# Kernel tuning notes

Hardware: AMD Instinct MI355X
Metric: run time of the kernel (lower is better)

The kernel has to match this reference:

```python
import jax, jax.numpy as jnp
import numpy as np

H, L, N = 512, 2048, 64  # channels, seq len, SSM state size


def _make_dplr_hippo(n):
    # make_HiPPO / make_NPLR_HiPPO / make_DPLR_HiPPO from the source
    p0 = np.sqrt(1.0 + 2.0 * np.arange(n))
    A = p0[:, None] * p0[None, :]
    A = np.tril(A) - np.diag(np.arange(n))
    nhippo = -A
    P = np.sqrt(np.arange(n) + 0.5)
    B = np.sqrt(2.0 * np.arange(n) + 1.0)
    S = nhippo + P[:, None] * P[None, :]
    S_diag = np.diagonal(S)
    Lam_re = np.mean(S_diag) * np.ones_like(S_diag)
    Lam_im, V = jnp.linalg.eigh(jnp.asarray(S, jnp.complex64) * (-1j))
    Pc = V.conj().T @ jnp.asarray(P, jnp.complex64)
    Bc = V.conj().T @ jnp.asarray(B, jnp.complex64)
    return (jnp.asarray(Lam_re, jnp.float32), jnp.asarray(Lam_im, jnp.float32),
            Pc, Bc)


def setup_inputs() -> dict:
    key = jax.random.key(0)
    k_u, k_c, k_s = jax.random.split(key, 3)
    Lre, Lim, Pc, Bc = _make_dplr_hippo(N)
    tile = lambda v: jnp.tile(v[None, :], (H, 1)).astype(jnp.float32)  # (H,N)
    return {
        "u": jax.random.normal(k_u, (L, H), dtype=jnp.float32),
        "x0_re": jnp.zeros((N, H), jnp.float32),
        "x0_im": jnp.zeros((N, H), jnp.float32),
        "Lambda_re": tile(Lre),
        "Lambda_im": tile(Lim),
        "P_re": tile(Pc.real), "P_im": tile(Pc.imag),
        "B_re": tile(Bc.real), "B_im": tile(Bc.imag),
        "C": jax.random.normal(k_c, (H, N, 2), jnp.float32) * (0.5 ** 0.5),
        "D": jnp.ones((H, 1), jnp.float32),
        "log_step": jax.random.uniform(k_s, (H, 1), jnp.float32,
                                       minval=np.log(1e-3), maxval=np.log(1e-1)),
    }


def _discretize(Lam, P, B, Ct, step):
    # discrete_DPLR with Q = P (as in setup); per-channel, vmapped over H.
    n = Lam.shape[0]
    I = jnp.eye(n, dtype=jnp.complex64)
    A = jnp.diag(Lam) - P[:, None] * P.conj()[None, :]
    A0 = (2.0 / step) * I + A
    Dd = jnp.diag(1.0 / (2.0 / step - Lam))
    Qc = P.conj()[None, :]            # (1,N)
    P2 = P[:, None]                   # (N,1)
    A1 = Dd - (Dd @ P2) * (1.0 / (1.0 + Qc @ Dd @ P2)) * (Qc @ Dd)
    Ab = A1 @ A0                      # (N,N)
    Bb = 2.0 * (A1 @ B[:, None])[:, 0]
    AbL = jnp.linalg.matrix_power(Ab, L)
    Cb = (Ct[None, :] @ jnp.linalg.inv(I - AbL).conj()).conj()[0]
    return Ab, Bb, Cb


def _forward(u, x0_re, x0_im, Lambda_re, Lambda_im, P_re, P_im,
             B_re, B_im, C, D, log_step):
    Lam = jnp.clip(Lambda_re, None, -0.0001) + 1j * Lambda_im  # (H,N)
    Pc = P_re + 1j * P_im
    Bc = B_re + 1j * B_im
    Cc = C[..., 0] + 1j * C[..., 1]
    step = jnp.exp(log_step)[:, 0]                              # (H,)
    Ab, Bb, Cb = jax.vmap(_discretize)(Lam, Pc, Bc, Cc, step)   # (H,N,N),(H,N),(H,N)

    x0 = jnp.transpose(x0_re + 1j * x0_im)                      # (H,N) complex

    def body(x, u_t):  # x: (H,N) complex, u_t: (H,)
        x = jnp.einsum('hnm,hm->hn', Ab, x) + Bb * u_t[:, None]
        y = jnp.einsum('hn,hn->h', Cb, x)
        return x, y.real

    _, ys = jax.lax.scan(body, x0, u)                           # ys: (L,H)
    return ys + u * D[:, 0][None, :]                            # (L,H) float32


def reference(u, x0_re, x0_im, Lambda_re, Lambda_im, P_re, P_im,
              B_re, B_im, C, D, log_step):
    return _forward(u, x0_re, x0_im, Lambda_re, Lambda_im, P_re, P_im,
                    B_re, B_im, C, D, log_step)
```

## Files before the change

kernel.cpp:

```cpp
#include <hip/hip_runtime.h>

#define HH 512
#define LL 2048
#define NN 64
#define TT 64
#define CC 32
#define NLDA 68
#define SP 72

typedef __attribute__((ext_vector_type(8))) short bf16x8_t;
typedef __attribute__((ext_vector_type(4))) float floatx4;

__device__ __forceinline__ float2 cmul(float2 a, float2 b) {
    return make_float2(a.x * b.x - a.y * b.y, a.x * b.y + a.y * b.x);
}
__device__ __forceinline__ float2 crecip(float2 a) {
    float id = 1.0f / (a.x * a.x + a.y * a.y);
    return make_float2(a.x * id, -a.y * id);
}
template <int CTRL>
__device__ __forceinline__ float dpp_mov(float x) {
    return __int_as_float(__builtin_amdgcn_update_dpp(
        0, __float_as_int(x), CTRL, 0xf, 0xf, true));
}
__device__ __forceinline__ float wave_sum_bcast(float x) {
    x += dpp_mov<0x111>(x);
    x += dpp_mov<0x112>(x);
    x += dpp_mov<0x114>(x);
    x += dpp_mov<0x118>(x);
    x += dpp_mov<0x142>(x);
    x += dpp_mov<0x143>(x);
    return __int_as_float(__builtin_amdgcn_readlane(__float_as_int(x), 63));
}
__device__ __forceinline__ float rlane(float x, int i) {
    return __int_as_float(__builtin_amdgcn_readlane(__float_as_int(x), i));
}
__device__ __forceinline__ unsigned short f2bf(float f) {
    unsigned int u = __float_as_uint(f);
    u += 0x7FFFu + ((u >> 16) & 1u);
    return (unsigned short)(u >> 16);
}
__device__ __forceinline__ float bf2f(unsigned short s) {
    return __uint_as_float(((unsigned int)s) << 16);
}

__device__ __forceinline__ void closed_form(
    int h, int n,
    const float* __restrict__ Lre, const float* __restrict__ Lim,
    const float* __restrict__ Pre, const float* __restrict__ Pim,
    const float* __restrict__ Bre, const float* __restrict__ Bim,
    const float* __restrict__ logstep,
    float2& da, float2& DPv, float2& tv, float2& bb) {
    float step = expf(logstep[h]);
    float as = 2.0f / step;
    float lr = fminf(Lre[h * NN + n], -1e-4f);
    float li = Lim[h * NN + n];
    float2 a = make_float2(as + lr, li);
    float2 Dn = crecip(make_float2(as - lr, -li));
    float2 P = make_float2(Pre[h * NN + n], Pim[h * NN + n]);
    float2 Bv = make_float2(Bre[h * NN + n], Bim[h * NN + n]);
    float2 cP = make_float2(P.x, -P.y);
    float p2 = P.x * P.x + P.y * P.y;
    float2 rt = cmul(cmul(cP, Dn), Bv);
    float2 e = make_float2(wave_sum_bcast(Dn.x * p2), wave_sum_bcast(Dn.y * p2));
    float2 rv = make_float2(wave_sum_bcast(rt.x), wave_sum_bcast(rt.y));
    float2 cc = crecip(make_float2(1.0f + e.x, e.y));
    da = cmul(Dn, a);
    DPv = cmul(Dn, P);
    float2 tmp = cmul(cc, make_float2(da.x - e.x, da.y - e.y));
    tv = cmul(cP, make_float2(1.0f + tmp.x, tmp.y));
    float2 crv = cmul(cc, rv);
    float2 cd = cmul(crv, DPv);
    float2 db = cmul(Dn, Bv);
    bb = make_float2(2.0f * (db.x - cd.x), 2.0f * (db.y - cd.y));
}

__device__ __forceinline__ void pack_tiles(
    unsigned short* mRh, unsigned short* mRl,
    unsigned short* mIh, unsigned short* mIl,
    unsigned short* mTRh, unsigned short* mTRl,
    unsigned short* mTIh, unsigned short* mTIl,
    int w, int lm, int q, const float Cr[4][4], const float Ci[4][4]) {
    #pragma unroll
    for (int nt = 0; nt < 4; ++nt) {
        const int c = nt * 16 + lm;
        unsigned short hr[4], lr_[4], hi_[4], li_[4];
        #pragma unroll
        for (int reg = 0; reg < 4; ++reg) {
            const float xr = Cr[nt][reg], xi = Ci[nt][reg];
            hr[reg] = f2bf(xr); lr_[reg] = f2bf(xr - bf2f(hr[reg]));
            hi_[reg] = f2bf(xi); li_[reg] = f2bf(xi - bf2f(hi_[reg]));
            const int r = 16 * w + 4 * q + reg;
            mRh[r * SP + c] = hr[reg]; mRl[r * SP + c] = lr_[reg];
            mIh[r * SP + c] = hi_[reg]; mIl[r * SP + c] = li_[reg];
        }
        const int tb = c * SP + 16 * w + 4 * q;
        *(ushort4*)&mTRh[tb] = make_ushort4(hr[0], hr[1], hr[2], hr[3]);
        *(ushort4*)&mTRl[tb] = make_ushort4(lr_[0], lr_[1], lr_[2], lr_[3]);
        *(ushort4*)&mTIh[tb] = make_ushort4(hi_[0], hi_[1], hi_[2], hi_[3]);
        *(ushort4*)&mTIl[tb] = make_ushort4(li_[0], li_[1], li_[2], li_[3]);
    }
}

extern "C" __global__ void __launch_bounds__(256, 2)
k_fusedA(const float* __restrict__ Lre, const float* __restrict__ Lim,
         const float* __restrict__ Pre, const float* __restrict__ Pim,
         const float* __restrict__ Bre, const float* __restrict__ Bim,
         const float* __restrict__ Cmat, const float* __restrict__ logstep,
         const float* __restrict__ u,
         float2* __restrict__ wM, float2* __restrict__ wCb,
         float2* __restrict__ wP) {
    extern __shared__ __align__(16) char smem[];
    const int tid = threadIdx.x;

    if (blockIdx.x < HH) {
        const int h = blockIdx.x;
        unsigned short* mRh  = (unsigned short*)smem;
        unsigned short* mRl  = mRh + 64 * SP;
        unsigned short* mIh  = mRl + 64 * SP;
        unsigned short* mIl  = mIh + 64 * SP;
        unsigned short* mTRh = mIl + 64 * SP;
        unsigned short* mTRl = mTRh + 64 * SP;
        unsigned short* mTIh = mTRl + 64 * SP;
        unsigned short* mTIl = mTIh + 64 * SP;
        float* Nr = (float*)smem;
        float* Ni = Nr + 64 * NLDA;
        float2* sda  = (float2*)(smem + 73728);
        float2* sDP  = sda + NN;
        float2* st   = sDP + NN;
        float2* sBb  = st + NN;
        float2* srhs = sBb + NN;
        float2* sx   = srhs + NN;
        float2* pp   = sx + NN;

        const int w = tid >> 6;
        const int lane = tid & 63;
        const int lm = lane & 15, q = lane >> 4;

        if (tid < NN) {
            float2 da, DPv, tv, bb;
            closed_form(h, tid, Lre, Lim, Pre, Pim, Bre, Bim, logstep,
                        da, DPv, tv, bb);
            sda[tid] = da; sDP[tid] = DPv; st[tid] = tv; sBb[tid] = bb;
            srhs[tid] = make_float2(Cmat[h * NN * 2 + tid * 2],
                                    -Cmat[h * NN * 2 + tid * 2 + 1]);
        }
        __syncthreads();

        {
            float Cr[4][4], Ci[4][4];
            #pragma unroll
            for (int nt = 0; nt < 4; ++nt) {
                const int c = nt * 16 + lm;
                const float2 tc = st[c];
                #pragma unroll
                for (int reg = 0; reg < 4; ++reg) {
                    const int r = 16 * w + 4 * q + reg;
                    const float2 dp = sDP[r];
                    float vr = -(dp.x * tc.x - dp.y * tc.y);
                    float vi = -(dp.x * tc.y + dp.y * tc.x);
                    if (r == c) { vr += sda[r].x; vi += sda[r].y; }
                    Cr[nt][reg] = vr; Ci[nt][reg] = vi;
                }
            }
            pack_tiles(mRh, mRl, mIh, mIl, mTRh, mTRl, mTIh, mTIl,
                       w, lm, q, Cr, Ci);
        }
        __syncthreads();

        const int arow = (16 * w + lm) * SP + q * 8;
        for (int it = 0; it < 11; ++it) {
            floatx4 z4 = {0.f, 0.f, 0.f, 0.f};
            floatx4 aP[4] = {z4, z4, z4, z4};
            floatx4 aQ[4] = {z4, z4, z4, z4};
            floatx4 aC[4] = {z4, z4, z4, z4};
            for (int k2 = 0; k2 < 2; ++k2) {
                const int ao = arow + k2 * 32;
                const bf16x8_t ARh = *(const bf16x8_t*)&mRh[ao];
                const bf16x8_t ARl = *(const bf16x8_t*)&mRl[ao];
                const bf16x8_t AIh = *(const bf16x8_t*)&mIh[ao];
                const bf16x8_t AIl = *(const bf16x8_t*)&mIl[ao];
                bf16x8_t BRh[4], BRl[4], BIh[4], BIl[4];
                #pragma unroll
                for (int nt = 0; nt < 4; ++nt) {
                    const int bo = (nt * 16 + lm) * SP + k2 * 32 + q * 8;
                    BRh[nt] = *(const bf16x8_t*)&mTRh[bo];
                    BRl[nt] = *(const bf16x8_t*)&mTRl[bo];
                    BIh[nt] = *(const bf16x8_t*)&mTIh[bo];
                    BIl[nt] = *(const bf16x8_t*)&mTIl[bo];
                }
                #pragma unroll
                for (int nt = 0; nt < 4; ++nt) {
                    aP[nt] = __builtin_amdgcn_mfma_f32_16x16x32_bf16(ARh, BRh[nt], aP[nt], 0, 0, 0);
                    aP[nt] = __builtin_amdgcn_mfma_f32_16x16x32_bf16(ARh, BRl[nt], aP[nt], 0, 0, 0);
                    aP[nt] = __builtin_amdgcn_mfma_f32_16x16x32_bf16(ARl, BRh[nt], aP[nt], 0, 0, 0);
                    aQ[nt] = __builtin_amdgcn_mfma_f32_16x16x32_bf16(AIh, BIh[nt], aQ[nt], 0, 0, 0);
                    aQ[nt] = __builtin_amdgcn_mfma_f32_16x16x32_bf16(AIh, BIl[nt], aQ[nt], 0, 0, 0);
                    aQ[nt] = __builtin_amdgcn_mfma_f32_16x16x32_bf16(AIl, BIh[nt], aQ[nt], 0, 0, 0);
                    aC[nt] = __builtin_amdgcn_mfma_f32_16x16x32_bf16(ARh, BIh[nt], aC[nt], 0, 0, 0);
                    aC[nt] = __builtin_amdgcn_mfma_f32_16x16x32_bf16(ARh, BIl[nt], aC[nt], 0, 0, 0);
                    aC[nt] = __builtin_amdgcn_mfma_f32_16x16x32_bf16(ARl, BIh[nt], aC[nt], 0, 0, 0);
                    aC[nt] = __builtin_amdgcn_mfma_f32_16x16x32_bf16(AIh, BRh[nt], aC[nt], 0, 0, 0);
                    aC[nt] = __builtin_amdgcn_mfma_f32_16x16x32_bf16(AIh, BRl[nt], aC[nt], 0, 0, 0);
                    aC[nt] = __builtin_amdgcn_mfma_f32_16x16x32_bf16(AIl, BRh[nt], aC[nt], 0, 0, 0);
                }
            }
            __syncthreads();
            if (it < 10) {
                float Cr[4][4], Ci[4][4];
                #pragma unroll
                for (int nt = 0; nt < 4; ++nt)
                    #pragma unroll
                    for (int reg = 0; reg < 4; ++reg) {
                        Cr[nt][reg] = aP[nt][reg] - aQ[nt][reg];
                        Ci[nt][reg] = aC[nt][reg];
                    }
                pack_tiles(mRh, mRl, mIh, mIl, mTRh, mTRl, mTIh, mTIl,
                           w, lm, q, Cr, Ci);
                __syncthreads();
                if (it == 5) {
                    for (int idx = tid; idx < NN * NN; idx += 256) {
                        const int c = idx >> 6, k = idx & 63;
                        wM[h * NN * NN + idx] = make_float2(
                            bf2f(mTRh[c * SP + k]) + bf2f(mTRl[c * SP + k]),
                            bf2f(mTIh[c * SP + k]) + bf2f(mTIl[c * SP + k]));
                    }
                }
            } else {
                #pragma unroll
                for (int nt = 0; nt < 4; ++nt) {
                    const int c = nt * 16 + lm;
                    #pragma unroll
                    for (int reg = 0; reg < 4; ++reg) {
                        const int r = 16 * w + 4 * q + reg;
                        Nr[r * NLDA + c] = aP[nt][reg] - aQ[nt][reg];
                        Ni[r * NLDA + c] = aC[nt][reg];
                    }
                }
                __syncthreads();
            }
        }

        if (tid < NN) sx[tid] = srhs[tid];
        __syncthreads();
        for (int itn = 0; itn < 24; ++itn) {
            const int i = tid & 63, qq = tid >> 6;
            float pr = 0.0f, pi = 0.0f;
            #pragma unroll 4
            for (int jj = 0; jj < 16; ++jj) {
                const int j = qq * 16 + jj;
                const float nr = Nr[j * NLDA + i], ni = Ni[j * NLDA + i];
                const float2 xj = sx[j];
                pr += nr * xj.x - ni * xj.y;
                pi += nr * xj.y + ni * xj.x;
            }
            pp[qq * 64 + i] = make_float2(pr, pi);
            __syncthreads();
            if (tid < NN) {
                const float2 a0 = pp[tid], a1 = pp[64 + tid];
                const float2 a2 = pp[128 + tid], a3 = pp[192 + tid];
                sx[tid] = make_float2(
                    srhs[tid].x + a0.x + a1.x + a2.x + a3.x,
                    srhs[tid].y + a0.y + a1.y + a2.y + a3.y);
            }
            __syncthreads();
        }
        if (tid < NN) wCb[h * NN + tid] = sx[tid];
    } else {
        const int h = blockIdx.x - HH;
        float2* sG  = (float2*)smem;
        float*  su  = (float*)(smem + 32768);
        float2* sda = (float2*)(smem + 40960);
        float2* sDP = sda + NN;
        float2* st  = sDP + NN;
        float2* sBb = st + NN;

        const int wv = tid >> 6, lane = tid & 63;
        for (int idx = tid; idx < LL; idx += 256)
            su[idx] = u[idx * HH + h];
        if (tid < NN) {
            float2 da, DPv, tv, bb;
            closed_form(h, tid, Lre, Lim, Pre, Pim, Bre, Bim, logstep,
                        da, DPv, tv, bb);
            sda[tid] = da; sDP[tid] = DPv; st[tid] = tv; sBb[tid] = bb;
        }
        __syncthreads();

        if (tid < 64) {
            const float2 da = sda[lane], DP = sDP[lane], tt = st[lane];
            float Gr = sBb[lane].x, Gi = sBb[lane].y;
            for (int m = 0; m < TT; ++m) {
                sG[m * NN + lane] = make_float2(Gr, Gi);
                float c1 = tt.x * Gr - tt.y * Gi;
                float c2 = tt.x * Gi + tt.y * Gr;
                c1 += dpp_mov<0x111>(c1); c2 += dpp_mov<0x111>(c2);
                c1 += dpp_mov<0x112>(c1); c2 += dpp_mov<0x112>(c2);
                c1 += dpp_mov<0x114>(c1); c2 += dpp_mov<0x114>(c2);
                c1 += dpp_mov<0x118>(c1); c2 += dpp_mov<0x118>(c2);
                c1 += dpp_mov<0x142>(c1); c2 += dpp_mov<0x142>(c2);
                c1 += dpp_mov<0x143>(c1); c2 += dpp_mov<0x143>(c2);
                const float S1 = rlane(c1, 63);
                const float S2 = rlane(c2, 63);
                float nGr = da.x * Gr - da.y * Gi - (DP.x * S1 - DP.y * S2);
                float nGi = da.x * Gi + da.y * Gr - (DP.x * S2 + DP.y * S1);
                Gr = nGr; Gi = nGi;
            }
        }
        __syncthreads();

        float accr[8] = {}, acci[8] = {};
        for (int j = 0; j < TT; ++j) {
            const float2 g = sG[(TT - 1 - j) * NN + lane];
            #pragma unroll
            for (int qc = 0; qc < 8; ++qc) {
                const float uv = su[((wv * 8 + qc) << 6) + j];
                accr[qc] += g.x * uv; acci[qc] += g.y * uv;
            }
        }
        #pragma unroll
        for (int qc = 0; qc < 8; ++qc)
            wP[(h * CC + wv * 8 + qc) * NN + lane] = make_float2(accr[qc], acci[qc]);
    }
}

extern "C" __global__ void __launch_bounds__(256, 2)
k_fusedB(const float* __restrict__ Lre, const float* __restrict__ Lim,
         const float* __restrict__ Pre, const float* __restrict__ Pim,
         const float* __restrict__ Bre, const float* __restrict__ Bim,
         const float* __restrict__ logstep,
         const float* __restrict__ u, const float* __restrict__ Dvec,
         const float* __restrict__ x0_re, const float* __restrict__ x0_im,
         const float2* __restrict__ wM, const float2* __restrict__ wCb,
         const float2* __restrict__ wP, float* __restrict__ out) {
    extern __shared__ __align__(16) char smem[];
    float2* sM          = (float2*)smem;
    unsigned short* sVr = (unsigned short*)(smem + 32768);
    unsigned short* sVi = (unsigned short*)(smem + 41216);
    float2* sXs         = (float2*)(smem + 49664);
    float*  su          = (float*)(smem + 66048);
    float*  sK          = (float*)(smem + 74240);

    const int h = blockIdx.x;
    const int tid = threadIdx.x;
    const int wv = tid >> 6, lane = tid & 63;

    for (int idx = tid; idx < NN * NN; idx += 256)
        sM[idx] = wM[h * NN * NN + idx];
    for (int idx = tid; idx < LL; idx += 256)
        su[idx] = u[idx * HH + h];
    __syncthreads();

    if (wv == 0) {
        float2 da, DP, tt, Bb;
        closed_form(h, lane, Lre, Lim, Pre, Pim, Bre, Bim, logstep,
                    da, DP, tt, Bb);
        const float2 Cb = wCb[h * NN + lane];
        float Gr = Bb.x, Gi = Bb.y;
        float vr = Cb.x, vi = Cb.y;
        for (int m = 0; m < TT; ++m) {
            float ch[5];
            ch[0] = Cb.x * Gr - Cb.y * Gi;
            ch[1] = tt.x * Gr - tt.y * Gi;
            ch[2] = tt.x * Gi + tt.y * Gr;
            ch[3] = vr * DP.x - vi * DP.y;
            ch[4] = vr * DP.y + vi * DP.x;
            #pragma unroll
            for (int c = 0; c < 5; ++c) ch[c] += dpp_mov<0x111>(ch[c]);
            #pragma unroll
            for (int c = 0; c < 5; ++c) ch[c] += dpp_mov<0x112>(ch[c]);
            #pragma unroll
            for (int c = 0; c < 5; ++c) ch[c] += dpp_mov<0x114>(ch[c]);
            #pragma unroll
            for (int c = 0; c < 5; ++c) ch[c] += dpp_mov<0x118>(ch[c]);
            #pragma unroll
            for (int c = 0; c < 5; ++c) ch[c] += dpp_mov<0x142>(ch[c]);
            #pragma unroll
            for (int c = 0; c < 5; ++c) ch[c] += dpp_mov<0x143>(ch[c]);
            const float S0 = rlane(ch[0], 63);
            const float S1 = rlane(ch[1], 63);
            const float S2 = rlane(ch[2], 63);
            const float S3 = rlane(ch[3], 63);
            const float S4 = rlane(ch[4], 63);
            if (lane == 0) sK[m] = S0;
            float nGr = da.x * Gr - da.y * Gi - (DP.x * S1 - DP.y * S2);
            float nGi = da.x * Gi + da.y * Gr - (DP.x * S2 + DP.y * S1);
            Gr = nGr; Gi = nGi;
            float nvr = da.x * vr - da.y * vi - (S3 * tt.x - S4 * tt.y);
            float nvi = da.x * vi + da.y * vr - (S3 * tt.y + S4 * tt.x);
            vr = nvr; vi = nvi;
            sVr[lane * 66 + m] = f2bf(vr);
            sVi[lane * 66 + m] = f2bf(vi);
        }
    } else if (wv == 1) {
        float xr = x0_re[lane * HH + h], xi = x0_im[lane * HH + h];
        sXs[lane] = make_float2(xr, xi);
        for (int c = 1; c < CC; ++c) {
            float nr = 0.0f, ni = 0.0f;
            #pragma unroll 8
            for (int j = 0; j < NN; ++j) {
                const float xjr = rlane(xr, j);
                const float xji = rlane(xi, j);
                const float2 m = sM[j * NN + lane];
                nr += m.x * xjr - m.y * xji;
                ni += m.x * xji + m.y * xjr;
            }
            const float2 pe = wP[(h * CC + (c - 1)) * NN + lane];
            xr = nr + pe.x; xi = ni + pe.y;
            sXs[c * NN + lane] = make_float2(xr, xi);
        }
    }
    __syncthreads();

    const float Dh = Dvec[h];
    const int t = lane;
    float acc[8] = {};
    for (int s = 0; s < TT; ++s) {
        const int d = t - s;
        const float kv = (d >= 0) ? sK[d < 0 ? 0 : d] : 0.0f;
        #pragma unroll
        for (int qc = 0; qc < 8; ++qc)
            acc[qc] += kv * su[((wv * 8 + qc) << 6) + s];
    }
    for (int n = 0; n < NN; ++n) {
        const float vvr = bf2f(sVr[n * 66 + t]);
        const float vvi = bf2f(sVi[n * 66 + t]);
        #pragma unroll
        for (int qc = 0; qc < 8; ++qc) {
            const float2 xs = sXs[(wv * 8 + qc) * NN + n];
            acc[qc] += vvr * xs.x - vvi * xs.y;
        }
    }
    #pragma unroll
    for (int qc = 0; qc < 8; ++qc) {
        const int c = wv * 8 + qc;
        out[(c * TT + t) * HH + h] = acc[qc] + Dh * su[c * TT + t];
    }
}

extern "C" void kernel_launch(void* const* d_in, const int* in_sizes, int n_in,
                              void* d_out, int out_size, void* d_ws, size_t ws_size,
                              hipStream_t stream) {
    const float* u    = (const float*)d_in[0];
    const float* x0re = (const float*)d_in[1];
    const float* x0im = (const float*)d_in[2];
    const float* Lre  = (const float*)d_in[3];
    const float* Lim  = (const float*)d_in[4];
    const float* Pre  = (const float*)d_in[5];
    const float* Pim  = (const float*)d_in[6];
    const float* Bre  = (const float*)d_in[7];
    const float* Bim  = (const float*)d_in[8];
    const float* C    = (const float*)d_in[9];
    const float* Dv   = (const float*)d_in[10];
    const float* lst  = (const float*)d_in[11];

    float2* wM  = (float2*)d_ws;
    float2* wP  = wM + HH * NN * NN;
    float2* wCb = wP + HH * CC * NN;
    float* out = (float*)d_out;

    hipLaunchKernelGGL(k_fusedA, dim3(2 * HH), dim3(256), 78848, stream,
                       Lre, Lim, Pre, Pim, Bre, Bim, C, lst, u,
                       wM, wCb, wP);
    hipLaunchKernelGGL(k_fusedB, dim3(HH), dim3(256), 74496, stream,
                       Lre, Lim, Pre, Pim, Bre, Bim, lst, u, Dv,
                       x0re, x0im, wM, wCb, wP, out);
}
```

Measured before the change: 233.9 us.

## Fuse discretization, chunk-input and scan kernels into one per-channel kernel

Merges the two launches into a single kernel of 512 blocks, one per channel. The G/P chunk-input blocks and the output kernel are folded into the matrix-power block, so Cb, the chunk inputs P and the closed-form parameters stay in shared memory instead of round-tripping through global workspace. The chunk-to-chunk state propagation now reads the M matrix directly from global memory (written earlier by the same block) rather than staging it in shared memory. This halves the grid and serializes work that previously ran in parallel blocks, and it risks slower M reads from global memory in the sequential chunk recurrence.

New measurement: 255.2 us. +9.1%, slower.

```diff
diff --git a/kernel.cpp b/kernel.cpp
--- a/kernel.cpp
+++ b/kernel.cpp
@@ -7,6 +7,7 @@
 #define CC 32
 #define NLDA 68
 #define SP 72
+
 
 typedef __attribute__((ext_vector_type(8))) short bf16x8_t;
 typedef __attribute__((ext_vector_type(4))) float floatx4;
@@ -103,259 +104,182 @@
 }
 
 extern "C" __global__ void __launch_bounds__(256, 2)
-k_fusedA(const float* __restrict__ Lre, const float* __restrict__ Lim,
-         const float* __restrict__ Pre, const float* __restrict__ Pim,
-         const float* __restrict__ Bre, const float* __restrict__ Bim,
-         const float* __restrict__ Cmat, const float* __restrict__ logstep,
-         const float* __restrict__ u,
-         float2* __restrict__ wM, float2* __restrict__ wCb,
-         float2* __restrict__ wP) {
+k_all(const float* __restrict__ Lre, const float* __restrict__ Lim,
+      const float* __restrict__ Pre, const float* __restrict__ Pim,
+      const float* __restrict__ Bre, const float* __restrict__ Bim,
+      const float* __restrict__ Cmat, const float* __restrict__ logstep,
+      const float* __restrict__ u, const float* __restrict__ Dvec,
+      const float* __restrict__ x0_re, const float* __restrict__ x0_im,
+      float2* __restrict__ wM, float* __restrict__ out) {
     extern __shared__ __align__(16) char smem[];
     const int tid = threadIdx.x;
-
-    if (blockIdx.x < HH) {
-        const int h = blockIdx.x;
-        unsigned short* mRh  = (unsigned short*)smem;
-        unsigned short* mRl  = mRh + 64 * SP;
-        unsigned short* mIh  = mRl + 64 * SP;
-        unsigned short* mIl  = mIh + 64 * SP;
-        unsigned short* mTRh = mIl + 64 * SP;
-        unsigned short* mTRl = mTRh + 64 * SP;
-        unsigned short* mTIh = mTRl + 64 * SP;
-        unsigned short* mTIl = mTIh + 64 * SP;
-        float* Nr = (float*)smem;
-        float* Ni = Nr + 64 * NLDA;
-        float2* sda  = (float2*)(smem + 73728);
-        float2* sDP  = sda + NN;
-        float2* st   = sDP + NN;
-        float2* sBb  = st + NN;
-        float2* srhs = sBb + NN;
-        float2* sx   = srhs + NN;
-        float2* pp   = sx + NN;
-
-        const int w = tid >> 6;
-        const int lane = tid & 63;
-        const int lm = lane & 15, q = lane >> 4;
-
-        if (tid < NN) {
-            float2 da, DPv, tv, bb;
-            closed_form(h, tid, Lre, Lim, Pre, Pim, Bre, Bim, logstep,
-                        da, DPv, tv, bb);
-            sda[tid] = da; sDP[tid] = DPv; st[tid] = tv; sBb[tid] = bb;
-            srhs[tid] = make_float2(Cmat[h * NN * 2 + tid * 2],
-                                    -Cmat[h * NN * 2 + tid * 2 + 1]);
+    const int h = blockIdx.x;
+
+    unsigned short* mRh  = (unsigned short*)smem;
+    unsigned short* mRl  = mRh + 64 * SP;
+    unsigned short* mIh  = mRl + 64 * SP;
+    unsigned short* mIl  = mIh + 64 * SP;
+    unsigned short* mTRh = mIl + 64 * SP;
+    unsigned short* mTRl = mTRh + 64 * SP;
+    unsigned short* mTIh = mTRl + 64 * SP;
+    unsigned short* mTIl = mTIh + 64 * SP;
+    float* Nr = (float*)smem;
+    float* Ni = Nr + 64 * NLDA;
+    float2* sda  = (float2*)(smem + 74240);
+    float2* sDP  = sda + NN;
+    float2* st   = sDP + NN;
+    float2* sBb  = st + NN;
+    float2* srhs = sBb + NN;
+    float2* sx   = srhs + NN;
+    float2* pp   = sx + NN;
+    float2* sG   = (float2*)smem;
+    unsigned short* sVr = (unsigned short*)(smem + 32768);
+    unsigned short* sVi = (unsigned short*)(smem + 41216);
+    float2* sP   = (float2*)(smem + 49664);
+    float*  su   = (float*)(smem + 66048);
+    float*  sK   = (float*)srhs;
+    float2* sXs  = (float2*)smem;
+
+    const int w = tid >> 6;
+    const int lane = tid & 63;
+    const int lm = lane & 15, q = lane >> 4;
+    const int wv = w;
+
+    if (tid < NN) {
+        float2 da, DPv, tv, bb;
+        closed_form(h, tid, Lre, Lim, Pre, Pim, Bre, Bim, logstep,
+                    da, DPv, tv, bb);
+        sda[tid] = da; sDP[tid] = DPv; st[tid] = tv; sBb[tid] = bb;
+        srhs[tid] = make_float2(Cmat[h * NN * 2 + tid * 2],
+                                -Cmat[h * NN * 2 + tid * 2 + 1]);
+    }
+    __syncthreads();
+
+    {
+        float Cr[4][4], Ci[4][4];
+        #pragma unroll
+        for (int nt = 0; nt < 4; ++nt) {
+            const int c = nt * 16 + lm;
+            const float2 tc = st[c];
+            #pragma unroll
+            for (int reg = 0; reg < 4; ++reg) {
+                const int r = 16 * w + 4 * q + reg;
+                const float2 dp = sDP[r];
+                float vr = -(dp.x * tc.x - dp.y * tc.y);
+                float vi = -(dp.x * tc.y + dp.y * tc.x);
+                if (r == c) { vr += sda[r].x; vi += sda[r].y; }
+                Cr[nt][reg] = vr; Ci[nt][reg] = vi;
+            }
+        }
+        pack_tiles(mRh, mRl, mIh, mIl, mTRh, mTRl, mTIh, mTIl,
+                   w, lm, q, Cr, Ci);
+    }
+    __syncthreads();
+
+    const int arow = (16 * w + lm) * SP + q * 8;
+    for (int it = 0; it < 11; ++it) {
+        floatx4 z4 = {0.f, 0.f, 0.f, 0.f};
+        floatx4 aP[4] = {z4, z4, z4, z4};
+        floatx4 aQ[4] = {z4, z4, z4, z4};
+        floatx4 aC[4] = {z4, z4, z4, z4};
+        for (int k2 = 0; k2 < 2; ++k2) {
+            const int ao = arow + k2 * 32;
+            const bf16x8_t ARh = *(const bf16x8_t*)&mRh[ao];
+            const bf16x8_t ARl = *(const bf16x8_t*)&mRl[ao];
+            const bf16x8_t AIh = *(const bf16x8_t*)&mIh[ao];
+            const bf16x8_t AIl = *(const bf16x8_t*)&mIl[ao];
+            bf16x8_t BRh[4], BRl[4], BIh[4], BIl[4];
+            #pragma unroll
+            for (int nt = 0; nt < 4; ++nt) {
+                const int bo = (nt * 16 + lm) * SP + k2 * 32 + q * 8;
+                BRh[nt] = *(const bf16x8_t*)&mTRh[bo];
+                BRl[nt] = *(const bf16x8_t*)&mTRl[bo];
+                BIh[nt] = *(const bf16x8_t*)&mTIh[bo];
+                BIl[nt] = *(const bf16x8_t*)&mTIl[bo];
+            }
+            #pragma unroll
+            for (int nt = 0; nt < 4; ++nt) {
+                aP[nt] = __builtin_amdgcn_mfma_f32_16x16x32_bf16(ARh, BRh[nt], aP[nt], 0, 0, 0);
+                aP[nt] = __builtin_amdgcn_mfma_f32_16x16x32_bf16(ARh, BRl[nt], aP[nt], 0, 0, 0);
+                aP[nt] = __builtin_amdgcn_mfma_f32_16x16x32_bf16(ARl, BRh[nt], aP[nt], 0, 0, 0);
+                aQ[nt] = __builtin_amdgcn_mfma_f32_16x16x32_bf16(AIh, BIh[nt], aQ[nt], 0, 0, 0);
+                aQ[nt] = __builtin_amdgcn_mfma_f32_16x16x32_bf16(AIh, BIl[nt], aQ[nt], 0, 0, 0);
+                aQ[nt] = __builtin_amdgcn_mfma_f32_16x16x32_bf16(AIl, BIh[nt], aQ[nt], 0, 0, 0);
+                aC[nt] = __builtin_amdgcn_mfma_f32_16x16x32_bf16(ARh, BIh[nt], aC[nt], 0, 0, 0);
+                aC[nt] = __builtin_amdgcn_mfma_f32_16x16x32_bf16(ARh, BIl[nt], aC[nt], 0, 0, 0);
+                aC[nt] = __builtin_amdgcn_mfma_f32_16x16x32_bf16(ARl, BIh[nt], aC[nt], 0, 0, 0);
+                aC[nt] = __builtin_amdgcn_mfma_f32_16x16x32_bf16(AIh, BRh[nt], aC[nt], 0, 0, 0);
+                aC[nt] = __builtin_amdgcn_mfma_f32_16x16x32_bf16(AIh, BRl[nt], aC[nt], 0, 0, 0);
+                aC[nt] = __builtin_amdgcn_mfma_f32_16x16x32_bf16(AIl, BRh[nt], aC[nt], 0, 0, 0);
+            }
         }
         __syncthreads();
-
-        {
+        if (it < 10) {
             float Cr[4][4], Ci[4][4];
+            #pragma unroll
+            for (int nt = 0; nt < 4; ++nt)
+                #pragma unroll
+                for (int reg = 0; reg < 4; ++reg) {
+                    Cr[nt][reg] = aP[nt][reg] - aQ[nt][reg];
+                    Ci[nt][reg] = aC[nt][reg];
+                }
+            pack_tiles(mRh, mRl, mIh, mIl, mTRh, mTRl, mTIh, mTIl,
+                       w, lm, q, Cr, Ci);
+            __syncthreads();
+            if (it == 5) {
+                for (int idx = tid; idx < NN * NN; idx += 256) {
+                    const int c = idx >> 6, k = idx & 63;
+                    wM[h * NN * NN + idx] = make_float2(
+                        bf2f(mTRh[c * SP + k]) + bf2f(mTRl[c * SP + k]),
+                        bf2f(mTIh[c * SP + k]) + bf2f(mTIl[c * SP + k]));
+                }
+            }
+        } else {
             #pragma unroll
             for (int nt = 0; nt < 4; ++nt) {
                 const int c = nt * 16 + lm;
-                const float2 tc = st[c];
                 #pragma unroll
                 for (int reg = 0; reg < 4; ++reg) {
                     const int r = 16 * w + 4 * q + reg;
-                    const float2 dp = sDP[r];
-                    float vr = -(dp.x * tc.x - dp.y * tc.y);
-                    float vi = -(dp.x * tc.y + dp.y * tc.x);
-                    if (r == c) { vr += sda[r].x; vi += sda[r].y; }
-                    Cr[nt][reg] = vr; Ci[nt][reg] = vi;
+                    Nr[r * NLDA + c] = aP[nt][reg] - aQ[nt][reg];
+                    Ni[r * NLDA + c] = aC[nt][reg];
                 }
             }
-            pack_tiles(mRh, mRl, mIh, mIl, mTRh, mTRl, mTIh, mTIl,
-                       w, lm, q, Cr, Ci);
-        }
+            for (int idx = tid; idx < LL; idx += 256)
+                su[idx] = u[idx * HH + h];
+            __syncthreads();
+        }
+    }
+
+    if (tid < NN) sx[tid] = srhs[tid];
+    __syncthreads();
+    for (int itn = 0; itn < 24; ++itn) {
+        const int i = tid & 63, qq = tid >> 6;
+        float pr = 0.0f, pi = 0.0f;
+        #pragma unroll 4
+        for (int jj = 0; jj < 16; ++jj) {
+            const int j = qq * 16 + jj;
+            const float nr = Nr[j * NLDA + i], ni = Ni[j * NLDA + i];
+            const float2 xj = sx[j];
+            pr += nr * xj.x - ni * xj.y;
+            pi += nr * xj.y + ni * xj.x;
+        }
+        pp[qq * 64 + i] = make_float2(pr, pi);
         __syncthreads();
-
-        const int arow = (16 * w + lm) * SP + q * 8;
-        for (int it = 0; it < 11; ++it) {
-            floatx4 z4 = {0.f, 0.f, 0.f, 0.f};
-            floatx4 aP[4] = {z4, z4, z4, z4};
-            floatx4 aQ[4] = {z4, z4, z4, z4};
-            floatx4 aC[4] = {z4, z4, z4, z4};
-            for (int k2 = 0; k2 < 2; ++k2) {
-                const int ao = arow + k2 * 32;
-                const bf16x8_t ARh = *(const bf16x8_t*)&mRh[ao];
-                const bf16x8_t ARl = *(const bf16x8_t*)&mRl[ao];
-                const bf16x8_t AIh = *(const bf16x8_t*)&mIh[ao];
-                const bf16x8_t AIl = *(const bf16x8_t*)&mIl[ao];
-                bf16x8_t BRh[4], BRl[4], BIh[4], BIl[4];
-                #pragma unroll
-                for (int nt = 0; nt < 4; ++nt) {
-                    const int bo = (nt * 16 + lm) * SP + k2 * 32 + q * 8;
-                    BRh[nt] = *(const bf16x8_t*)&mTRh[bo];
-                    BRl[nt] = *(const bf16x8_t*)&mTRl[bo];
-                    BIh[nt] = *(const bf16x8_t*)&mTIh[bo];
-                    BIl[nt] = *(const bf16x8_t*)&mTIl[bo];
-                }
-                #pragma unroll
-                for (int nt = 0; nt < 4; ++nt) {
-                    aP[nt] = __builtin_amdgcn_mfma_f32_16x16x32_bf16(ARh, BRh[nt], aP[nt], 0, 0, 0);
-                    aP[nt] = __builtin_amdgcn_mfma_f32_16x16x32_bf16(ARh, BRl[nt], aP[nt], 0, 0, 0);
-                    aP[nt] = __builtin_amdgcn_mfma_f32_16x16x32_bf16(ARl, BRh[nt], aP[nt], 0, 0, 0);
-                    aQ[nt] = __builtin_amdgcn_mfma_f32_16x16x32_bf16(AIh, BIh[nt], aQ[nt], 0, 0, 0);
-                    aQ[nt] = __builtin_amdgcn_mfma_f32_16x16x32_bf16(AIh, BIl[nt], aQ[nt], 0, 0, 0);
-                    aQ[nt] = __builtin_amdgcn_mfma_f32_16x16x32_bf16(AIl, BIh[nt], aQ[nt], 0, 0, 0);
-                    aC[nt] = __builtin_amdgcn_mfma_f32_16x16x32_bf16(ARh, BIh[nt], aC[nt], 0, 0, 0);
-                    aC[nt] = __builtin_amdgcn_mfma_f32_16x16x32_bf16(ARh, BIl[nt], aC[nt], 0, 0, 0);
-                    aC[nt] = __builtin_amdgcn_mfma_f32_16x16x32_bf16(ARl, BIh[nt], aC[nt], 0, 0, 0);
-                    aC[nt] = __builtin_amdgcn_mfma_f32_16x16x32_bf16(AIh, BRh[nt], aC[nt], 0, 0, 0);
-                    aC[nt] = __builtin_amdgcn_mfma_f32_16x16x32_bf16(AIh, BRl[nt], aC[nt], 0, 0, 0);
-                    aC[nt] = __builtin_amdgcn_mfma_f32_16x16x32_bf16(AIl, BRh[nt], aC[nt], 0, 0, 0);
-                }
-            }
-            __syncthreads();
-            if (it < 10) {
-                float Cr[4][4], Ci[4][4];
-                #pragma unroll
-                for (int nt = 0; nt < 4; ++nt)
-                    #pragma unroll
-                    for (int reg = 0; reg < 4; ++reg) {
-                        Cr[nt][reg] = aP[nt][reg] - aQ[nt][reg];
-                        Ci[nt][reg] = aC[nt][reg];
-                    }
-                pack_tiles(mRh, mRl, mIh, mIl, mTRh, mTRl, mTIh, mTIl,
-                           w, lm, q, Cr, Ci);
-                __syncthreads();
-                if (it == 5) {
-                    for (int idx = tid; idx < NN * NN; idx += 256) {
-                        const int c = idx >> 6, k = idx & 63;
-                        wM[h * NN * NN + idx] = make_float2(
-                            bf2f(mTRh[c * SP + k]) + bf2f(mTRl[c * SP + k]),
-                            bf2f(mTIh[c * SP + k]) + bf2f(mTIl[c * SP + k]));
-                    }
-                }
-            } else {
-                #pragma unroll
-                for (int nt = 0; nt < 4; ++nt) {
-                    const int c = nt * 16 + lm;
-                    #pragma unroll
-                    for (int reg = 0; reg < 4; ++reg) {
-                        const int r = 16 * w + 4 * q + reg;
-                        Nr[r * NLDA + c] = aP[nt][reg] - aQ[nt][reg];
-                        Ni[r * NLDA + c] = aC[nt][reg];
-                    }
-                }
-                __syncthreads();
-            }
-        }
-
-        if (tid < NN) sx[tid] = srhs[tid];
+        if (tid < NN) {
+            const float2 a0 = pp[tid], a1 = pp[64 + tid];
+            const float2 a2 = pp[128 + tid], a3 = pp[192 + tid];
+            sx[tid] = make_float2(
+                srhs[tid].x + a0.x + a1.x + a2.x + a3.x,
+                srhs[tid].y + a0.y + a1.y + a2.y + a3.y);
+        }
         __syncthreads();
-        for (int itn = 0; itn < 24; ++itn) {
-            const int i = tid & 63, qq = tid >> 6;
-            float pr = 0.0f, pi = 0.0f;
-            #pragma unroll 4
-            for (int jj = 0; jj < 16; ++jj) {
-                const int j = qq * 16 + jj;
-                const float nr = Nr[j * NLDA + i], ni = Ni[j * NLDA + i];
-                const float2 xj = sx[j];
-                pr += nr * xj.x - ni * xj.y;
-                pi += nr * xj.y + ni * xj.x;
-            }
-            pp[qq * 64 + i] = make_float2(pr, pi);
-            __syncthreads();
-            if (tid < NN) {
-                const float2 a0 = pp[tid], a1 = pp[64 + tid];
-                const float2 a2 = pp[128 + tid], a3 = pp[192 + tid];
-                sx[tid] = make_float2(
-                    srhs[tid].x + a0.x + a1.x + a2.x + a3.x,
-                    srhs[tid].y + a0.y + a1.y + a2.y + a3.y);
-            }
-            __syncthreads();
-        }
-        if (tid < NN) wCb[h * NN + tid] = sx[tid];
-    } else {
-        const int h = blockIdx.x - HH;
-        float2* sG  = (float2*)smem;
-        float*  su  = (float*)(smem + 32768);
-        float2* sda = (float2*)(smem + 40960);
-        float2* sDP = sda + NN;
-        float2* st  = sDP + NN;
-        float2* sBb = st + NN;
-
-        const int wv = tid >> 6, lane = tid & 63;
-        for (int idx = tid; idx < LL; idx += 256)
-            su[idx] = u[idx * HH + h];
-        if (tid < NN) {
-            float2 da, DPv, tv, bb;
-            closed_form(h, tid, Lre, Lim, Pre, Pim, Bre, Bim, logstep,
-                        da, DPv, tv, bb);
-            sda[tid] = da; sDP[tid] = DPv; st[tid] = tv; sBb[tid] = bb;
-        }
-        __syncthreads();
-
-        if (tid < 64) {
-            const float2 da = sda[lane], DP = sDP[lane], tt = st[lane];
-            float Gr = sBb[lane].x, Gi = sBb[lane].y;
-            for (int m = 0; m < TT; ++m) {
-                sG[m * NN + lane] = make_float2(Gr, Gi);
-                float c1 = tt.x * Gr - tt.y * Gi;
-                float c2 = tt.x * Gi + tt.y * Gr;
-                c1 += dpp_mov<0x111>(c1); c2 += dpp_mov<0x111>(c2);
-                c1 += dpp_mov<0x112>(c1); c2 += dpp_mov<0x112>(c2);
-                c1 += dpp_mov<0x114>(c1); c2 += dpp_mov<0x114>(c2);
-                c1 += dpp_mov<0x118>(c1); c2 += dpp_mov<0x118>(c2);
-                c1 += dpp_mov<0x142>(c1); c2 += dpp_mov<0x142>(c2);
-                c1 += dpp_mov<0x143>(c1); c2 += dpp_mov<0x143>(c2);
-                const float S1 = rlane(c1, 63);
-                const float S2 = rlane(c2, 63);
-                float nGr = da.x * Gr - da.y * Gi - (DP.x * S1 - DP.y * S2);
-                float nGi = da.x * Gi + da.y * Gr - (DP.x * S2 + DP.y * S1);
-                Gr = nGr; Gi = nGi;
-            }
-        }
-        __syncthreads();
-
-        float accr[8] = {}, acci[8] = {};
-        for (int j = 0; j < TT; ++j) {
-            const float2 g = sG[(TT - 1 - j) * NN + lane];
-            #pragma unroll
-            for (int qc = 0; qc < 8; ++qc) {
-                const float uv = su[((wv * 8 + qc) << 6) + j];
-                accr[qc] += g.x * uv; acci[qc] += g.y * uv;
-            }
-        }
-        #pragma unroll
-        for (int qc = 0; qc < 8; ++qc)
-            wP[(h * CC + wv * 8 + qc) * NN + lane] = make_float2(accr[qc], acci[qc]);
-    }
-}
-
-extern "C" __global__ void __launch_bounds__(256, 2)
-k_fusedB(const float* __restrict__ Lre, const float* __restrict__ Lim,
-         const float* __restrict__ Pre, const float* __restrict__ Pim,
-         const float* __restrict__ Bre, const float* __restrict__ Bim,
-         const float* __restrict__ logstep,
-         const float* __restrict__ u, const float* __restrict__ Dvec,
-         const float* __restrict__ x0_re, const float* __restrict__ x0_im,
-         const float2* __restrict__ wM, const float2* __restrict__ wCb,
-         const float2* __restrict__ wP, float* __restrict__ out) {
-    extern __shared__ __align__(16) char smem[];
-    float2* sM          = (float2*)smem;
-    unsigned short* sVr = (unsigned short*)(smem + 32768);
-    unsigned short* sVi = (unsigned short*)(smem + 41216);
-    float2* sXs         = (float2*)(smem + 49664);
-    float*  su          = (float*)(smem + 66048);
-    float*  sK          = (float*)(smem + 74240);
-
-    const int h = blockIdx.x;
-    const int tid = threadIdx.x;
-    const int wv = tid >> 6, lane = tid & 63;
-
-    for (int idx = tid; idx < NN * NN; idx += 256)
-        sM[idx] = wM[h * NN * NN + idx];
-    for (int idx = tid; idx < LL; idx += 256)
-        su[idx] = u[idx * HH + h];
-    __syncthreads();
+    }
 
     if (wv == 0) {
-        float2 da, DP, tt, Bb;
-        closed_form(h, lane, Lre, Lim, Pre, Pim, Bre, Bim, logstep,
-                    da, DP, tt, Bb);
-        const float2 Cb = wCb[h * NN + lane];
-        float Gr = Bb.x, Gi = Bb.y;
+        const float2 Cb = sx[lane];
+        const float2 da = sda[lane], DP = sDP[lane], tt = st[lane];
+        float Gr = sBb[lane].x, Gi = sBb[lane].y;
         float vr = Cb.x, vi = Cb.y;
         for (int m = 0; m < TT; ++m) {
             float ch[5];
@@ -392,6 +316,44 @@
             sVi[lane * 66 + m] = f2bf(vi);
         }
     } else if (wv == 1) {
+        const float2 da = sda[lane], DP = sDP[lane], tt = st[lane];
+        float Gr = sBb[lane].x, Gi = sBb[lane].y;
+        for (int m = 0; m < TT; ++m) {
+            sG[m * NN + lane] = make_float2(Gr, Gi);
+            float c1 = tt.x * Gr - tt.y * Gi;
+            float c2 = tt.x * Gi + tt.y * Gr;
+            c1 += dpp_mov<0x111>(c1); c2 += dpp_mov<0x111>(c2);
+            c1 += dpp_mov<0x112>(c1); c2 += dpp_mov<0x112>(c2);
+            c1 += dpp_mov<0x114>(c1); c2 += dpp_mov<0x114>(c2);
+            c1 += dpp_mov<0x118>(c1); c2 += dpp_mov<0x118>(c2);
+            c1 += dpp_mov<0x142>(c1); c2 += dpp_mov<0x142>(c2);
+            c1 += dpp_mov<0x143>(c1); c2 += dpp_mov<0x143>(c2);
+            const float S1 = rlane(c1, 63);
+            const float S2 = rlane(c2, 63);
+            float nGr = da.x * Gr - da.y * Gi - (DP.x * S1 - DP.y * S2);
+            float nGi = da.x * Gi + da.y * Gr - (DP.x * S2 + DP.y * S1);
+            Gr = nGr; Gi = nGi;
+        }
+    }
+    __syncthreads();
+
+    {
+        float accr[8] = {}, acci[8] = {};
+        for (int j = 0; j < TT; ++j) {
+            const float2 g = sG[(TT - 1 - j) * NN + lane];
+            #pragma unroll
+            for (int qc = 0; qc < 8; ++qc) {
+                const float uv = su[((wv * 8 + qc) << 6) + j];
+                accr[qc] += g.x * uv; acci[qc] += g.y * uv;
+            }
+        }
+        #pragma unroll
+        for (int qc = 0; qc < 8; ++qc)
+            sP[(wv * 8 + qc) * NN + lane] = make_float2(accr[qc], acci[qc]);
+    }
+    __syncthreads();
+
+    if (wv == 1) {
         float xr = x0_re[lane * HH + h], xi = x0_im[lane * HH + h];
         sXs[lane] = make_float2(xr, xi);
         for (int c = 1; c < CC; ++c) {
@@ -400,40 +362,42 @@
             for (int j = 0; j < NN; ++j) {
                 const float xjr = rlane(xr, j);
                 const float xji = rlane(xi, j);
-                const float2 m = sM[j * NN + lane];
+                const float2 m = wM[h * NN * NN + j * NN + lane];
                 nr += m.x * xjr - m.y * xji;
                 ni += m.x * xji + m.y * xjr;
             }
-            const float2 pe = wP[(h * CC + (c - 1)) * NN + lane];
+            const float2 pe = sP[(c - 1) * NN + lane];
             xr = nr + pe.x; xi = ni + pe.y;
             sXs[c * NN + lane] = make_float2(xr, xi);
         }
     }
     __syncthreads();
 
-    const float Dh = Dvec[h];
-    const int t = lane;
-    float acc[8] = {};
-    for (int s = 0; s < TT; ++s) {
-        const int d = t - s;
-        const float kv = (d >= 0) ? sK[d < 0 ? 0 : d] : 0.0f;
-        #pragma unroll
-        for (int qc = 0; qc < 8; ++qc)
-            acc[qc] += kv * su[((wv * 8 + qc) << 6) + s];
-    }
-    for (int n = 0; n < NN; ++n) {
-        const float vvr = bf2f(sVr[n * 66 + t]);
-        const float vvi = bf2f(sVi[n * 66 + t]);
+    {
+        const float Dh = Dvec[h];
+        const int t = lane;
+        float acc[8] = {};
+        for (int s = 0; s < TT; ++s) {
+            const int d = t - s;
+            const float kv = (d >= 0) ? sK[d < 0 ? 0 : d] : 0.0f;
+            #pragma unroll
+            for (int qc = 0; qc < 8; ++qc)
+                acc[qc] += kv * su[((wv * 8 + qc) << 6) + s];
+        }
+        for (int n = 0; n < NN; ++n) {
+            const float vvr = bf2f(sVr[n * 66 + t]);
+            const float vvi = bf2f(sVi[n * 66 + t]);
+            #pragma unroll
+            for (int qc = 0; qc < 8; ++qc) {
+                const float2 xs = sXs[(wv * 8 + qc) * NN + n];
+                acc[qc] += vvr * xs.x - vvi * xs.y;
+            }
+        }
         #pragma unroll
         for (int qc = 0; qc < 8; ++qc) {
-            const float2 xs = sXs[(wv * 8 + qc) * NN + n];
-            acc[qc] += vvr * xs.x - vvi * xs.y;
-        }
-    }
-    #pragma unroll
-    for (int qc = 0; qc < 8; ++qc) {
-        const int c = wv * 8 + qc;
-        out[(c * TT + t) * HH + h] = acc[qc] + Dh * su[c * TT + t];
+            const int c = wv * 8 + qc;
+            out[(c * TT + t) * HH + h] = acc[qc] + Dh * su[c * TT + t];
+        }
     }
 }
 
@@ -453,15 +417,10 @@
     const float* Dv   = (const float*)d_in[10];
     const float* lst  = (const float*)d_in[11];
 
-    float2* wM  = (float2*)d_ws;
-    float2* wP  = wM + HH * NN * NN;
-    float2* wCb = wP + HH * CC * NN;
+    float2* wM = (float2*)d_ws;
     float* out = (float*)d_out;
 
-    hipLaunchKernelGGL(k_fusedA, dim3(2 * HH), dim3(256), 78848, stream,
-                       Lre, Lim, Pre, Pim, Bre, Bim, C, lst, u,
-                       wM, wCb, wP);
-    hipLaunchKernelGGL(k_fusedB, dim3(HH), dim3(256), 74496, stream,
-                       Lre, Lim, Pre, Pim, Bre, Bim, lst, u, Dv,
-                       x0re, x0im, wM, wCb, wP, out);
-}
+    hipLaunchKernelGGL(k_all, dim3(HH), dim3(256), 79360, stream,
+                       Lre, Lim, Pre, Pim, Bre, Bim, C, lst, u, Dv,
+                       x0re, x0im, wM, out);
+}
```
